# Kernel optimization log

Hardware: AMD Instinct MI355X
Metric: run time of the kernel (lower is better)

Reference implementation:

```python
import jax, jax.numpy as jnp
import numpy as np

B, D, H, W, K = 2, 128, 256, 256, 4
OFFSET_SCALE = 1.0
BN_EPS = 1e-5


def conv2d(x, w, b=None, pad='SAME'):
    y = jax.lax.conv_general_dilated(x, w, (1, 1), pad,
                                     dimension_numbers=('NCHW', 'OIHW', 'NCHW'))
    if b is not None:
        y = y + b[None, :, None, None]
    return y


def grid_sample_border(img, gx, gy):
    # img: (b,d,H,W); gx,gy: (b,K,H,W) normalized coords in [-1,1]
    # bilinear, padding_mode='border', align_corners=True
    b, d, h, w = img.shape
    x = jnp.clip((gx + 1.0) * 0.5 * (w - 1), 0.0, w - 1)
    y = jnp.clip((gy + 1.0) * 0.5 * (h - 1), 0.0, h - 1)
    x0f = jnp.floor(x); y0f = jnp.floor(y)
    wx = x - x0f; wy = y - y0f
    x0 = x0f.astype(jnp.int32); y0 = y0f.astype(jnp.int32)
    x1 = jnp.minimum(x0 + 1, w - 1); y1 = jnp.minimum(y0 + 1, h - 1)
    imgT = jnp.transpose(img, (0, 2, 3, 1))  # (b,H,W,d)
    bidx = jnp.arange(b)[:, None, None, None]  # broadcasts over (b,K,H,W)
    def gather(yi, xi):
        return imgT[bidx, yi, xi]  # (b,K,H,W,d)
    out = (gather(y0, x0) * ((1 - wx) * (1 - wy))[..., None]
           + gather(y0, x1) * (wx * (1 - wy))[..., None]
           + gather(y1, x0) * ((1 - wx) * wy)[..., None]
           + gather(y1, x1) * (wx * wy)[..., None])
    return out  # (b,K,H,W,d)


def setup_inputs() -> dict:
    key = jax.random.key(0)
    ks = jax.random.split(key, 6)
    return {
        'bev': jax.random.normal(ks[0], (B, D, H, W), jnp.float32),
        'offset_w': jax.random.normal(ks[1], (2 * K, D, 3, 3), jnp.float32) * 0.02,
        'offset_b': jax.random.normal(ks[2], (2 * K,), jnp.float32) * 0.02,
        'weight_w': jax.random.normal(ks[3], (K, D, 3, 3), jnp.float32) * 0.05,
        'weight_b': jnp.zeros((K,), jnp.float32),
        'proj_w': jax.random.normal(ks[4], (D, D, 1, 1), jnp.float32) * (1.0 / np.sqrt(D)),
        'bn_gamma': jnp.ones((D,), jnp.float32),
        'bn_beta': jnp.zeros((D,), jnp.float32),
    }


def reference(bev, offset_w, offset_b, weight_w, weight_b, proj_w, bn_gamma, bn_beta):
    b, d, h, w = bev.shape
    # per-pixel K offsets (pixels) and K attention weights
    offsets = conv2d(bev, offset_w, offset_b) * OFFSET_SCALE  # (b,2K,H,W)
    w_logits = conv2d(bev, weight_w, weight_b)                # (b,K,H,W)
    attn = jax.nn.softmax(w_logits, axis=1)                   # softmax over K
    # base grid: replicates torch meshgrid(xy) + transpose (requires H==W)
    xs = jnp.linspace(-1.0, 1.0, w)
    ys = jnp.linspace(-1.0, 1.0, h)
    base_x = xs[:, None] * jnp.ones((1, h), jnp.float32)  # base_x[i,j] = xs[i]
    base_y = jnp.ones((w, 1), jnp.float32) * ys[None, :]  # base_y[i,j] = ys[j]
    off = offsets.reshape(b, K, 2, h, w)
    dx = off[:, :, 0]  # (b,K,H,W)
    dy = off[:, :, 1]
    dx_n = dx * (2.0 / (w - 1)) if w > 1 else dx * 0.0
    dy_n = dy * (2.0 / (h - 1)) if h > 1 else dy * 0.0
    gx = base_x[None, None] + dx_n  # (b,K,H,W)
    gy = base_y[None, None] + dy_n
    sampled = grid_sample_border(bev, gx, gy)  # (b,K,H,W,d)
    aggregated = jnp.einsum('bkhwd,bkhw->bdhw', sampled, attn)
    # proj: 1x1 conv (no bias) + BatchNorm2d (training mode: batch stats) + GELU(exact)
    y = conv2d(aggregated, proj_w)
    mean = jnp.mean(y, axis=(0, 2, 3), keepdims=True)
    var = jnp.mean((y - mean) ** 2, axis=(0, 2, 3), keepdims=True)
    y = (y - mean) * jax.lax.rsqrt(var + BN_EPS)
    y = y * bn_gamma[None, :, None, None] + bn_beta[None, :, None, None]
    return jax.nn.gelu(y, approximate=False)
```

## Files before the change

### kernel.cpp

```cpp
#include <hip/hip_runtime.h>
#include <math.h>

#define BB 2
#define DD 128
#define HH 256
#define WW 256
#define KK 4
#define HWC (HH*WW)
#define SROW2 320

typedef unsigned int u32;
typedef unsigned short ushort;
typedef __attribute__((ext_vector_type(8))) short bf16x8;
typedef __attribute__((ext_vector_type(4))) float f32x4;

#define OA_OFF    0
#define WTT_OFF   1572864
#define WP_OFF    1589248
#define STATS_OFF 1603072
#define PART_OFF  1603392
#define BEVT_OFF  1605440
#define PACC_OFF  18382656
#define PART2_OFF PACC_OFF
#define WBF_OFF   26771264
#define WCB_OFF   26779456
#define WS_NEED_BEVT  ((size_t)PACC_OFF * 4)
#define WS_NEED_FULL3 ((size_t)(WCB_OFF + 9216) * 4)

__device__ __forceinline__ u32 f2bf(float x) {
    u32 u = __builtin_bit_cast(u32, x);
    return (u + 0x7fffu + ((u >> 16) & 1u)) >> 16;
}
__device__ __forceinline__ u32 pkbf(float a, float b) {
    return f2bf(a) | (f2bf(b) << 16);
}
__device__ __forceinline__ float bflo(u32 d) { return __builtin_bit_cast(float, d << 16); }
__device__ __forceinline__ float bfhi(u32 d) { return __builtin_bit_cast(float, d & 0xffff0000u); }

__global__ __launch_bounds__(256) void k0_prep(
    const float* __restrict__ projw, const float* __restrict__ offw,
    const float* __restrict__ wtw, float* __restrict__ wtT, float* __restrict__ wp)
{
    int idx = blockIdx.x * 256 + threadIdx.x;
    if (idx < 16384) {
        int d = idx >> 7, o = idx & 127;
        wtT[d * 128 + o] = projw[o * 128 + d];
    }
    if (idx < 13824) {
        int c = idx / 108; int r = idx % 108; int o = r / 9; int t = r % 9;
        wp[idx] = (o < 8) ? offw[(o*128 + c)*9 + t] : wtw[((o-8)*128 + c)*9 + t];
    }
}

__global__ __launch_bounds__(256) void k0bc(
    const float* __restrict__ projw, const float* __restrict__ offw,
    const float* __restrict__ wtw, ushort* __restrict__ wbf,
    ushort* __restrict__ wcb)
{
    int idx = blockIdx.x * 256 + threadIdx.x;
    if (idx < 16384) wbf[idx] = (ushort)f2bf(projw[idx]);
    if (idx < 18432) {
        int tap = idx >> 11;
        int rem = idx & 2047;
        int oo = rem >> 7, c = rem & 127;
        float v = 0.f;
        if (oo < 8)       v = offw[(oo*128 + c)*9 + tap];
        else if (oo < 12) v = wtw[((oo-8)*128 + c)*9 + tap];
        wcb[idx] = (ushort)f2bf(v);
    }
}

__global__ __launch_bounds__(256) void k2t_bf(
    const float* __restrict__ bev, ushort* __restrict__ bevtb)
{
    __shared__ float T[64 * 128];
    int tid = threadIdx.x;
    int bidx = blockIdx.x;
    int b = bidx >> 10;
    int rem = bidx & 1023;
    int yrow = rem >> 2;
    int x0 = (rem & 3) << 6;

    const float* src = bev + ((size_t)b * DD) * HWC + (size_t)yrow * WW + x0;
    #pragma unroll 4
    for (int k = 0; k < 32; k++) {
        int flat = k * 256 + tid;
        int d = flat >> 6, xl = flat & 63;
        float v = src[(size_t)d * HWC + xl];
        T[xl * 128 + (((d >> 2) ^ (xl & 31)) << 2) + (d & 3)] = v;
    }
    __syncthreads();
    ushort* dst = bevtb + (((size_t)b * HH + yrow) * WW + x0) * 128;
    #pragma unroll 4
    for (int k = 0; k < 8; k++) {
        int flat = k * 256 + tid;
        int d4 = flat & 31, xl = (flat >> 5) & 63;
        float4 v = *(const float4*)&T[xl * 128 + ((d4 ^ (xl & 31)) << 2)];
        uint2 pk;
        pk.x = pkbf(v.x, v.y);
        pk.y = pkbf(v.z, v.w);
        *(uint2*)(dst + (size_t)xl * 128 + (d4 << 2)) = pk;
    }
}

__global__ __launch_bounds__(256) void k1m_conv_mfma(
    const ushort* __restrict__ bevtb, const ushort* __restrict__ wcb,
    const float* __restrict__ offb, const float* __restrict__ wtb,
    float* __restrict__ oa)
{
    __shared__ uint4 lds4[3168];

    int tid = threadIdx.x;
    int wv = tid >> 6;
    int l = tid & 63;
    int lm = l & 15, lk = l >> 4;
    int wgid = blockIdx.x;
    int lin = (wgid & 7) * 256 + (wgid >> 3);
    int b = lin >> 10;
    int i = (lin >> 2) & 255;
    int jt = lin & 3;
    int x0 = jt * 64;

    const ushort* bb = bevtb + (size_t)b * HWC * 128;
    for (int z = tid; z < 3168; z += 256) {
        int row = z / 1056;
        int rem = z - row * 1056;
        int pl = rem >> 4;
        int q  = rem & 15;
        int yy = i - 1 + row;
        int x  = x0 - 1 + pl;
        bool ok = ((unsigned)yy < HH) && ((unsigned)x < WW);
        uint4 v = make_uint4(0u, 0u, 0u, 0u);
        if (ok) v = *(const uint4*)(bb + ((size_t)(yy * WW + x) << 7) + q * 8);
        lds4[row * 1056 + pl * 16 + (q ^ (pl & 15))] = v;
    }
    __syncthreads();

    f32x4 acc = (f32x4)(0.f);
    #pragma unroll
    for (int dy = 0; dy < 3; dy++) {
        #pragma unroll
        for (int dx = 0; dx < 3; dx++) {
            int pl = wv * 16 + lm + dx;
            const uint4* bp = &lds4[dy * 1056 + pl * 16];
            int sx = pl & 15;
            const ushort* ap = wcb + (size_t)((dy*3 + dx) * 16 + lm) * 128 + lk * 8;
            #pragma unroll
            for (int kk = 0; kk < 4; kk++) {
                bf16x8 bfr = *(const bf16x8*)&bp[(kk*4 + lk) ^ sx];
                bf16x8 afr = *(const bf16x8*)(ap + kk * 32);
                acc = __builtin_amdgcn_mfma_f32_16x16x32_bf16(afr, bfr, acc, 0, 0, 0);
            }
        }
    }

    float v[4];
    #pragma unroll
    for (int r = 0; r < 4; r++) v[r] = acc[r];

    int j = x0 + wv * 16 + lm;
    if (lk < 2) {
        #pragma unroll
        for (int r = 0; r < 4; r++) v[r] += offb[lk*4 + r];
    } else if (lk == 2) {
        float l4[4];
        #pragma unroll
        for (int r = 0; r < 4; r++) l4[r] = v[r] + wtb[r];
        float m = fmaxf(fmaxf(l4[0], l4[1]), fmaxf(l4[2], l4[3]));
        float e[4]; float se = 0.f;
        #pragma unroll
        for (int r = 0; r < 4; r++) { e[r] = expf(l4[r] - m); se += e[r]; }
        float inv = 1.f / se;
        #pragma unroll
        for (int r = 0; r < 4; r++) v[r] = e[r] * inv;
    }
    if (lk < 3) {
        size_t basep = (size_t)b * 12 * HWC + (size_t)i * WW + j;
        #pragma unroll
        for (int r = 0; r < 4; r++)
            oa[basep + (size_t)(lk*4 + r) * HWC] = v[r];
    }
}

__global__ __launch_bounds__(256) void k2f_sample_proj(
    const ushort* __restrict__ bevtb, const float* __restrict__ oa,
    const ushort* __restrict__ wbf, float* __restrict__ y,
    float* __restrict__ part2)
{
    __shared__ uint4 P[32 * 16];

    int tid = threadIdx.x;
    int wgid = blockIdx.x;
    int lin = (wgid & 7) * 512 + (wgid >> 3);
    int b = lin >> 11;
    int pix0 = (lin & 2047) << 5;

    int q8 = tid & 7;
    int pixl = tid >> 3;
    int pix = pix0 + pixl;
    int p = pix >> 8;
    int q = pix & 255;

    const float* ob = oa + (size_t)b * 12 * HWC + (size_t)p * WW + q;
    unsigned pa[8]; float cw[16];
    #pragma unroll
    for (int k = 0; k < 4; k++) {
        float dx = ob[(size_t)(2*k)   * HWC];
        float dy = ob[(size_t)(2*k+1) * HWC];
        float a  = ob[(size_t)(8+k)   * HWC];
        float x  = fminf(fmaxf((float)p + dx, 0.f), (float)(WW-1));
        float yv = fminf(fmaxf((float)q + dy, 0.f), (float)(HH-1));
        float x0f = floorf(x); float y0f = floorf(yv);
        int x0 = (int)x0f; int y0 = (int)y0f;
        int x1 = min(x0 + 1, WW - 1); int y1 = min(y0 + 1, HH - 1);
        float wx = x - x0f; float wy = yv - y0f;
        pa[k*2+0] = (unsigned)(y0*WW + x0) | ((unsigned)(y0*WW + x1) << 16);
        pa[k*2+1] = (unsigned)(y1*WW + x0) | ((unsigned)(y1*WW + x1) << 16);
        cw[k*4+0] = a * (1.f - wx) * (1.f - wy);
        cw[k*4+1] = a * wx * (1.f - wy);
        cw[k*4+2] = a * (1.f - wx) * wy;
        cw[k*4+3] = a * wx * wy;
    }

    const ushort* bt = bevtb + (size_t)b * HWC * 128 + q8 * 8;

    float s[2][8];
    #pragma unroll
    for (int c = 0; c < 2; c++)
        #pragma unroll
        for (int e = 0; e < 8; e++) s[c][e] = 0.f;

    #pragma unroll
    for (int t = 0; t < 16; t++) {
        unsigned a01 = pa[t >> 1];
        unsigned gp = (t & 1) ? (a01 >> 16) : (a01 & 0xffffu);
        const ushort* tp = bt + ((size_t)gp << 7);
        float w = cw[t];
        #pragma unroll
        for (int c = 0; c < 2; c++) {
            uint4 v = *(const uint4*)(tp + c * 64);
            s[c][0] = fmaf(w, bflo(v.x), s[c][0]);
            s[c][1] = fmaf(w, bfhi(v.x), s[c][1]);
            s[c][2] = fmaf(w, bflo(v.y), s[c][2]);
            s[c][3] = fmaf(w, bfhi(v.y), s[c][3]);
            s[c][4] = fmaf(w, bflo(v.z), s[c][4]);
            s[c][5] = fmaf(w, bfhi(v.z), s[c][5]);
            s[c][6] = fmaf(w, bflo(v.w), s[c][6]);
            s[c][7] = fmaf(w, bfhi(v.w), s[c][7]);
        }
    }

    int sxr = pixl & 15;
    #pragma unroll
    for (int c = 0; c < 2; c++) {
        uint4 pk;
        pk.x = pkbf(s[c][0], s[c][1]);
        pk.y = pkbf(s[c][2], s[c][3]);
        pk.z = pkbf(s[c][4], s[c][5]);
        pk.w = pkbf(s[c][6], s[c][7]);
        P[pixl * 16 + ((c * 8 + q8) ^ sxr)] = pk;
    }
    __syncthreads();

    int wv = tid >> 6;
    int l = tid & 63;
    int lm = l & 15, lk = l >> 4;
    int o0 = wv << 5;

    f32x4 acc[2][2];
    #pragma unroll
    for (int ot = 0; ot < 2; ot++)
        #pragma unroll
        for (int nt = 0; nt < 2; nt++)
            acc[ot][nt] = (f32x4)(0.f);

    #pragma unroll
    for (int ot = 0; ot < 2; ot++) {
        const ushort* ap = wbf + (size_t)(o0 + ot * 16 + lm) * 128 + lk * 8;
        bf16x8 a4[4];
        #pragma unroll
        for (int kk = 0; kk < 4; kk++)
            a4[kk] = *(const bf16x8*)(ap + kk * 32);
        #pragma unroll
        for (int nt = 0; nt < 2; nt++) {
            int row = nt * 16 + lm;
            #pragma unroll
            for (int kk = 0; kk < 4; kk++) {
                bf16x8 bfr = *(const bf16x8*)&P[row * 16 + ((kk * 4 + lk) ^ lm)];
                acc[ot][nt] = __builtin_amdgcn_mfma_f32_16x16x32_bf16(
                    a4[kk], bfr, acc[ot][nt], 0, 0, 0);
            }
        }
    }

    #pragma unroll
    for (int ot = 0; ot < 2; ot++)
        #pragma unroll
        for (int nt = 0; nt < 2; nt++)
            #pragma unroll
            for (int r = 0; r < 4; r++)
                y[((size_t)b * DD + o0 + ot * 16 + lk * 4 + r) * HWC + pix0 + nt * 16 + lm]
                    = acc[ot][nt][r];

    float sm[2][4], sq[2][4];
    #pragma unroll
    for (int ot = 0; ot < 2; ot++)
        #pragma unroll
        for (int r = 0; r < 4; r++) { sm[ot][r] = 0.f; sq[ot][r] = 0.f; }
    #pragma unroll
    for (int ot = 0; ot < 2; ot++)
        #pragma unroll
        for (int nt = 0; nt < 2; nt++)
            #pragma unroll
            for (int r = 0; r < 4; r++) {
                float v = acc[ot][nt][r];
                sm[ot][r] += v;
                sq[ot][r] = fmaf(v, v, sq[ot][r]);
            }
    #pragma unroll
    for (int m = 1; m < 16; m <<= 1) {
        #pragma unroll
        for (int ot = 0; ot < 2; ot++)
            #pragma unroll
            for (int r = 0; r < 4; r++) {
                sm[ot][r] += __shfl_xor(sm[ot][r], m);
                sq[ot][r] += __shfl_xor(sq[ot][r], m);
            }
    }
    if (lm == 0) {
        #pragma unroll
        for (int ot = 0; ot < 2; ot++)
            #pragma unroll
            for (int r = 0; r < 4; r++) {
                int o = o0 + ot * 16 + lk * 4 + r;
                part2[(size_t)o * 4096 + wgid] = sm[ot][r];
                part2[(size_t)128 * 4096 + (size_t)o * 4096 + wgid] = sq[ot][r];
            }
    }
}

__global__ __launch_bounds__(256) void k3b_finalize2(
    const float* __restrict__ part2, const float* __restrict__ gamma,
    const float* __restrict__ beta, float* __restrict__ stats)
{
    int o = blockIdx.x; int tid = threadIdx.x;
    const float* ps = part2 + (size_t)o * 4096;
    const float* pq = part2 + (size_t)128 * 4096 + (size_t)o * 4096;
    double s = 0.0, s2 = 0.0;
    for (int i = tid; i < 4096; i += 256) { s += (double)ps[i]; s2 += (double)pq[i]; }
    __shared__ double ls[256], ls2[256];
    ls[tid] = s; ls2[tid] = s2;
    __syncthreads();
    for (int off = 128; off > 0; off >>= 1) {
        if (tid < off) { ls[tid] += ls[tid+off]; ls2[tid] += ls2[tid+off]; }
        __syncthreads();
    }
    if (tid == 0) {
        double N = (double)(BB * HWC);
        double mean = ls[0] / N;
        double var = ls2[0] / N - mean * mean;
        double invs = 1.0 / sqrt(var + 1e-5);
        double g = (double)gamma[o];
        stats[o*2]   = (float)(g * invs);
        stats[o*2+1] = (float)((double)beta[o] - mean * g * invs);
    }
}

__global__ __launch_bounds__(256) void k1_convs(
    const float* __restrict__ bev, const float* __restrict__ wp,
    const float* __restrict__ offb, const float* __restrict__ wtb,
    float* __restrict__ oa)
{
    __shared__ float rows[2][3][260];
    int tid = threadIdx.x;
    int p = blockIdx.x;
    int b = p / HH; int i = p % HH; int j = tid;
    const float* bb = bev + (size_t)b * DD * HWC;

    if (tid < 12) { int bf = tid / 6, r = tid % 6; rows[bf][r >> 1][(r & 1) ? 257 : 0] = 0.f; }
    #pragma unroll
    for (int l = 0; l < 3; l++) {
        int yy = i + l - 1;
        rows[0][l][1 + tid] = ((unsigned)yy < HH) ? bb[yy * WW + tid] : 0.f;
    }
    __syncthreads();

    float acc[12];
    #pragma unroll
    for (int o = 0; o < 12; o++) acc[o] = 0.f;

    for (int c = 0; c < 128; c++) {
        int cb = c & 1, nb = cb ^ 1;
        float rv[3];
        if (c < 127) {
            const float* pln = bb + (size_t)(c + 1) * HWC;
            #pragma unroll
            for (int l = 0; l < 3; l++) {
                int yy = i + l - 1;
                rv[l] = ((unsigned)yy < HH) ? pln[yy * WW + tid] : 0.f;
            }
        }
        float v[9];
        #pragma unroll
        for (int dy = 0; dy < 3; dy++)
            #pragma unroll
            for (int dx = 0; dx < 3; dx++)
                v[dy*3 + dx] = rows[cb][dy][tid + dx];
        const float* wc = wp + c * 108;
        #pragma unroll
        for (int o = 0; o < 12; o++) {
            float s = acc[o];
            #pragma unroll
            for (int t = 0; t < 9; t++) s = fmaf(wc[o*9 + t], v[t], s);
            acc[o] = s;
        }
        if (c < 127) {
            #pragma unroll
            for (int l = 0; l < 3; l++) rows[nb][l][1 + tid] = rv[l];
        }
        __syncthreads();
    }

    float outv[12];
    #pragma unroll
    for (int o = 0; o < 8; o++) outv[o] = acc[o] + offb[o];
    float l4[4];
    #pragma unroll
    for (int k = 0; k < 4; k++) l4[k] = acc[8+k] + wtb[k];
    float m = fmaxf(fmaxf(l4[0], l4[1]), fmaxf(l4[2], l4[3]));
    float e[4]; float se = 0.f;
    #pragma unroll
    for (int k = 0; k < 4; k++) { e[k] = expf(l4[k] - m); se += e[k]; }
    float inv = 1.f / se;
    #pragma unroll
    for (int k = 0; k < 4; k++) outv[8+k] = e[k] * inv;

    size_t basep = (size_t)b * 12 * HWC + (size_t)i * WW + j;
    #pragma unroll
    for (int o = 0; o < 12; o++) oa[basep + (size_t)o * HWC] = outv[o];
}

__global__ __launch_bounds__(256) void k2t_transpose(
    const float* __restrict__ bev, float* __restrict__ bevt)
{
    __shared__ float T[64 * 128];
    int tid = threadIdx.x;
    int bidx = blockIdx.x;
    int b = bidx >> 10;
    int rem = bidx & 1023;
    int yrow = rem >> 2;
    int x0 = (rem & 3) << 6;

    const float* src = bev + ((size_t)b * DD) * HWC + (size_t)yrow * WW + x0;
    #pragma unroll 4
    for (int k = 0; k < 32; k++) {
        int flat = k * 256 + tid;
        int d = flat >> 6, xl = flat & 63;
        float v = src[(size_t)d * HWC + xl];
        T[xl * 128 + (((d >> 2) ^ (xl & 31)) << 2) + (d & 3)] = v;
    }
    __syncthreads();
    float* dst = bevt + (((size_t)b * HH + yrow) * WW + x0) * 128;
    #pragma unroll 4
    for (int k = 0; k < 8; k++) {
        int flat = k * 256 + tid;
        int d4 = flat & 31, xl = (flat >> 5) & 63;
        float4 v = *(const float4*)&T[xl * 128 + ((d4 ^ (xl & 31)) << 2)];
        *(float4*)(dst + (size_t)xl * 128 + (d4 << 2)) = v;
    }
}

__global__ __launch_bounds__(512, 2) void k2_sample_proj_t(
    const float* __restrict__ bevt, const float* __restrict__ oa,
    const float* __restrict__ wt, float* __restrict__ y)
{
    __shared__ float S[2][16 * SROW2];

    int tid = threadIdx.x;
    int bidx = blockIdx.x;
    int b  = bidx >> 8;
    int p0 = ((bidx >> 4) & 15) * 16;
    int q0 = (bidx & 15) * 16;

    int gpix = tid >> 1;
    int gp = gpix & 15;
    int gq = gpix >> 4;
    int dgrp = tid & 1;
    int swr = gp * 20 + gq;

    int wv = tid >> 6;
    int wvu = __builtin_amdgcn_readfirstlane(wv);
    int lane = tid & 63;
    int lp = lane >> 2;
    int q4 = (lane & 3) << 2;
    int soff = lp * 20 + q4;

    const float* ob = oa + (size_t)b * 12 * HWC + (size_t)(p0 + gp) * WW + (q0 + gq);
    unsigned pa[8]; float cw[16];
    #pragma unroll
    for (int k = 0; k < 4; k++) {
        float dx = ob[(size_t)(2*k)   * HWC];
        float dy = ob[(size_t)(2*k+1) * HWC];
        float a  = ob[(size_t)(8+k)   * HWC];
        float x  = fminf(fmaxf((float)(p0 + gp) + dx, 0.f), (float)(WW-1));
        float yv = fminf(fmaxf((float)(q0 + gq) + dy, 0.f), (float)(HH-1));
        float x0f = floorf(x); float y0f = floorf(yv);
        int x0 = (int)x0f; int y0 = (int)y0f;
        int x1 = min(x0 + 1, WW - 1); int y1 = min(y0 + 1, HH - 1);
        float wx = x - x0f; float wy = yv - y0f;
        pa[k*2+0] = (unsigned)(y0*WW + x0) | ((unsigned)(y0*WW + x1) << 16);
        pa[k*2+1] = (unsigned)(y1*WW + x0) | ((unsigned)(y1*WW + x1) << 16);
        cw[k*4+0] = a * (1.f - wx) * (1.f - wy);
        cw[k*4+1] = a * wx * (1.f - wy);
        cw[k*4+2] = a * (1.f - wx) * wy;
        cw[k*4+3] = a * wx * wy;
    }

    const float* bt = bevt + (size_t)b * HWC * 128 + dgrp * 8;

    float acc[64];
    #pragma unroll
    for (int t = 0; t < 64; t++) acc[t] = 0.f;

    {
        float4 s0 = make_float4(0,0,0,0), s1 = make_float4(0,0,0,0);
        #pragma unroll
        for (int t = 0; t < 16; t++) {
            unsigned pix = (t & 1) ? (pa[t >> 1] >> 16) : (pa[t >> 1] & 0xffffu);
            const float4* tp = (const float4*)(bt + ((size_t)pix << 7));
            float4 va = tp[0], vb = tp[1];
            float c = cw[t];
            s0.x = fmaf(c, va.x, s0.x); s0.y = fmaf(c, va.y, s0.y);
            s0.z = fmaf(c, va.z, s0.z); s0.w = fmaf(c, va.w, s0.w);
            s1.x = fmaf(c, vb.x, s1.x); s1.y = fmaf(c, vb.y, s1.y);
            s1.z = fmaf(c, vb.z, s1.z); s1.w = fmaf(c, vb.w, s1.w);
        }
        int r = dgrp * 8;
        S[0][(r+0)*SROW2 + swr] = s0.x; S[0][(r+1)*SROW2 + swr] = s0.y;
        S[0][(r+2)*SROW2 + swr] = s0.z; S[0][(r+3)*SROW2 + swr] = s0.w;
        S[0][(r+4)*SROW2 + swr] = s1.x; S[0][(r+5)*SROW2 + swr] = s1.y;
        S[0][(r+6)*SROW2 + swr] = s1.z; S[0][(r+7)*SROW2 + swr] = s1.w;
    }
    __syncthreads();

    for (int c = 0; c < 8; c++) {
        int cur = c & 1;
        const float* Sc = &S[cur][0];
        float* Sn = &S[cur ^ 1][0];
        int d0 = c * 16;
        int dn = d0 + 16;
        bool more = (c < 7);

        float4 g0 = make_float4(0,0,0,0), g1 = make_float4(0,0,0,0);
        float4 pf0, pf1;
        if (more) {
            unsigned pix = pa[0] & 0xffffu;
            const float4* tp = (const float4*)(bt + ((size_t)pix << 7) + dn);
            pf0 = tp[0]; pf1 = tp[1];
        }

        #pragma unroll
        for (int dl = 0; dl < 16; dl++) {
            float4 cur0 = pf0, cur1 = pf1;
            if (more && dl < 15) {
                int t = dl + 1;
                unsigned pix = (t & 1) ? (pa[t >> 1] >> 16) : (pa[t >> 1] & 0xffffu);
                const float4* tp = (const float4*)(bt + ((size_t)pix << 7) + dn);
                pf0 = tp[0]; pf1 = tp[1];
            }

            float4 sv = *(const float4*)(Sc + dl * SROW2 + soff);
            const float4* wq = (const float4*)(wt + (size_t)(d0 + dl) * 128 + wvu * 16);
            #pragma unroll
            for (int oi4 = 0; oi4 < 4; oi4++) {
                float4 w4 = wq[oi4];
                int ob4 = oi4 * 16;
                acc[ob4+ 0] = fmaf(w4.x, sv.x, acc[ob4+ 0]);
                acc[ob4+ 1] = fmaf(w4.x, sv.y, acc[ob4+ 1]);
                acc[ob4+ 2] = fmaf(w4.x, sv.z, acc[ob4+ 2]);
                acc[ob4+ 3] = fmaf(w4.x, sv.w, acc[ob4+ 3]);
                acc[ob4+ 4] = fmaf(w4.y, sv.x, acc[ob4+ 4]);
                acc[ob4+ 5] = fmaf(w4.y, sv.y, acc[ob4+ 5]);
                acc[ob4+ 6] = fmaf(w4.y, sv.z, acc[ob4+ 6]);
                acc[ob4+ 7] = fmaf(w4.y, sv.w, acc[ob4+ 7]);
                acc[ob4+ 8] = fmaf(w4.z, sv.x, acc[ob4+ 8]);
                acc[ob4+ 9] = fmaf(w4.z, sv.y, acc[ob4+ 9]);
                acc[ob4+10] = fmaf(w4.z, sv.z, acc[ob4+10]);
                acc[ob4+11] = fmaf(w4.z, sv.w, acc[ob4+11]);
                acc[ob4+12] = fmaf(w4.w, sv.x, acc[ob4+12]);
                acc[ob4+13] = fmaf(w4.w, sv.y, acc[ob4+13]);
                acc[ob4+14] = fmaf(w4.w, sv.z, acc[ob4+14]);
                acc[ob4+15] = fmaf(w4.w, sv.w, acc[ob4+15]);
            }

            if (more) {
                float cwt = cw[dl];
                g0.x = fmaf(cwt, cur0.x, g0.x); g0.y = fmaf(cwt, cur0.y, g0.y);
                g0.z = fmaf(cwt, cur0.z, g0.z); g0.w = fmaf(cwt, cur0.w, g0.w);
                g1.x = fmaf(cwt, cur1.x, g1.x); g1.y = fmaf(cwt, cur1.y, g1.y);
                g1.z = fmaf(cwt, cur1.z, g1.z); g1.w = fmaf(cwt, cur1.w, g1.w);
            }
        }

        if (more) {
            int r = dgrp * 8;
            Sn[(r+0)*SROW2 + swr] = g0.x; Sn[(r+1)*SROW2 + swr] = g0.y;
            Sn[(r+2)*SROW2 + swr] = g0.z; Sn[(r+3)*SROW2 + swr] = g0.w;
            Sn[(r+4)*SROW2 + swr] = g1.x; Sn[(r+5)*SROW2 + swr] = g1.y;
            Sn[(r+6)*SROW2 + swr] = g1.z; Sn[(r+7)*SROW2 + swr] = g1.w;
        }
        __syncthreads();
    }

    size_t base = (size_t)b * DD * HWC + (size_t)(p0 + lp) * WW + (q0 + q4);
    #pragma unroll
    for (int oi = 0; oi < 16; oi++) {
        int o = wv * 16 + oi;
        float4 v = make_float4(acc[oi*4+0], acc[oi*4+1], acc[oi*4+2], acc[oi*4+3]);
        *(float4*)(y + base + (size_t)o * HWC) = v;
    }
}

__global__ __launch_bounds__(512, 2) void k2_sample_proj(
    const float* __restrict__ bev, const float* __restrict__ oa,
    const float* __restrict__ wt, float* __restrict__ y)
{
    __shared__ float S[2][16 * SROW2];
    int tid = threadIdx.x;
    int bidx = blockIdx.x;
    int b  = bidx >> 8;
    int p0 = ((bidx >> 4) & 15) * 16;
    int q0 = (bidx & 15) * 16;
    int pix = tid & 255;
    int gq = pix >> 4;
    int gp = pix & 15;
    int dgrp = tid >> 8;
    int swr = gp * 20 + gq;
    int wv = tid >> 6;
    int wvu = __builtin_amdgcn_readfirstlane(wv);
    int lane = tid & 63;
    int lp = lane >> 2;
    int q4 = (lane & 3) << 2;
    int soff = lp * 20 + q4;

    const float* ob = oa + (size_t)b * 12 * HWC + (size_t)(p0 + gp) * WW + (q0 + gq);
    unsigned pa[8]; float cw[16];
    #pragma unroll
    for (int k = 0; k < 4; k++) {
        float dx = ob[(size_t)(2*k)   * HWC];
        float dy = ob[(size_t)(2*k+1) * HWC];
        float a  = ob[(size_t)(8+k)   * HWC];
        float x  = fminf(fmaxf((float)(p0 + gp) + dx, 0.f), (float)(WW-1));
        float yv = fminf(fmaxf((float)(q0 + gq) + dy, 0.f), (float)(HH-1));
        float x0f = floorf(x); float y0f = floorf(yv);
        int x0 = (int)x0f; int y0 = (int)y0f;
        int x1 = min(x0 + 1, WW - 1); int y1 = min(y0 + 1, HH - 1);
        float wx = x - x0f; float wy = yv - y0f;
        pa[k*2+0] = (unsigned)(y0*WW + x0) | ((unsigned)(y0*WW + x1) << 16);
        pa[k*2+1] = (unsigned)(y1*WW + x0) | ((unsigned)(y1*WW + x1) << 16);
        cw[k*4+0] = a * (1.f - wx) * (1.f - wy);
        cw[k*4+1] = a * wx * (1.f - wy);
        cw[k*4+2] = a * (1.f - wx) * wy;
        cw[k*4+3] = a * wx * wy;
    }
    const float* bb = bev + (size_t)b * DD * HWC;
    float acc[64];
    #pragma unroll
    for (int t = 0; t < 64; t++) acc[t] = 0.f;
    #pragma unroll
    for (int dd = 0; dd < 8; dd++) {
        const float* pl = bb + (size_t)(dgrp*8 + dd) * HWC;
        float s = 0.f;
        #pragma unroll
        for (int t = 0; t < 8; t++) {
            unsigned a01 = pa[t];
            s = fmaf(cw[2*t],   pl[a01 & 0xffffu], s);
            s = fmaf(cw[2*t+1], pl[a01 >> 16], s);
        }
        S[0][(dgrp*8 + dd) * SROW2 + swr] = s;
    }
    __syncthreads();
    for (int c = 0; c < 8; c++) {
        int cur = c & 1;
        const float* Sc = &S[cur][0];
        float* Sn = &S[cur ^ 1][0];
        int d0 = c * 16;
        int d0n = d0 + 16;
        bool more = (c < 7);
        #pragma unroll
        for (int dl = 0; dl < 16; dl++) {
            if (dl < 8) {
                if (more) {
                    const float* pl = bb + (size_t)(d0n + dgrp*8 + dl) * HWC;
                    float s = 0.f;
                    #pragma unroll
                    for (int t = 0; t < 8; t++) {
                        unsigned a01 = pa[t];
                        s = fmaf(cw[2*t],   pl[a01 & 0xffffu], s);
                        s = fmaf(cw[2*t+1], pl[a01 >> 16], s);
                    }
                    Sn[(dgrp*8 + dl) * SROW2 + swr] = s;
                }
            }
            float4 sv = *(const float4*)(Sc + dl * SROW2 + soff);
            const float4* wq = (const float4*)(wt + (size_t)(d0 + dl) * 128 + wvu * 16);
            #pragma unroll
            for (int oi4 = 0; oi4 < 4; oi4++) {
                float4 w4 = wq[oi4];
                int ob4 = oi4 * 16;
                acc[ob4+ 0] = fmaf(w4.x, sv.x, acc[ob4+ 0]);
                acc[ob4+ 1] = fmaf(w4.x, sv.y, acc[ob4+ 1]);
                acc[ob4+ 2] = fmaf(w4.x, sv.z, acc[ob4+ 2]);
                acc[ob4+ 3] = fmaf(w4.x, sv.w, acc[ob4+ 3]);
                acc[ob4+ 4] = fmaf(w4.y, sv.x, acc[ob4+ 4]);
                acc[ob4+ 5] = fmaf(w4.y, sv.y, acc[ob4+ 5]);
                acc[ob4+ 6] = fmaf(w4.y, sv.z, acc[ob4+ 6]);
                acc[ob4+ 7] = fmaf(w4.y, sv.w, acc[ob4+ 7]);
                acc[ob4+ 8] = fmaf(w4.z, sv.x, acc[ob4+ 8]);
                acc[ob4+ 9] = fmaf(w4.z, sv.y, acc[ob4+ 9]);
                acc[ob4+10] = fmaf(w4.z, sv.z, acc[ob4+10]);
                acc[ob4+11] = fmaf(w4.z, sv.w, acc[ob4+11]);
                acc[ob4+12] = fmaf(w4.w, sv.x, acc[ob4+12]);
                acc[ob4+13] = fmaf(w4.w, sv.y, acc[ob4+13]);
                acc[ob4+14] = fmaf(w4.w, sv.z, acc[ob4+14]);
                acc[ob4+15] = fmaf(w4.w, sv.w, acc[ob4+15]);
            }
        }
        __syncthreads();
    }
    size_t base = (size_t)b * DD * HWC + (size_t)(p0 + lp) * WW + (q0 + q4);
    #pragma unroll
    for (int oi = 0; oi < 16; oi++) {
        int o = wv * 16 + oi;
        float4 v = make_float4(acc[oi*4+0], acc[oi*4+1], acc[oi*4+2], acc[oi*4+3]);
        *(float4*)(y + base + (size_t)o * HWC) = v;
    }
}

__global__ __launch_bounds__(256) void k3_partial(
    const float* __restrict__ y, double* __restrict__ part)
{
    int blk = blockIdx.x;
    int o = blk >> 2; int sub = blk & 3; int b = sub >> 1; int half = sub & 1;
    const float4* pl = (const float4*)(y + ((size_t)b * DD + o) * HWC + half * (HWC/2));
    int tid = threadIdx.x;
    double s = 0.0, s2 = 0.0;
    for (int idx = tid; idx < HWC/8; idx += 256) {
        float4 v = pl[idx];
        s  += (double)v.x + (double)v.y + (double)v.z + (double)v.w;
        s2 += (double)v.x*v.x + (double)v.y*v.y + (double)v.z*v.z + (double)v.w*v.w;
    }
    __shared__ double ls[256], ls2[256];
    ls[tid] = s; ls2[tid] = s2;
    __syncthreads();
    for (int off = 128; off > 0; off >>= 1) {
        if (tid < off) { ls[tid] += ls[tid+off]; ls2[tid] += ls2[tid+off]; }
        __syncthreads();
    }
    if (tid == 0) { part[blk*2] = ls[0]; part[blk*2+1] = ls2[0]; }
}

__global__ __launch_bounds__(128) void k3_finalize(
    const double* __restrict__ part, const float* __restrict__ gamma,
    const float* __restrict__ beta, float* __restrict__ stats)
{
    int o = threadIdx.x;
    double s = 0.0, s2 = 0.0;
    #pragma unroll
    for (int j = 0; j < 4; j++) { s += part[(o*4+j)*2]; s2 += part[(o*4+j)*2+1]; }
    double N = (double)(BB * HWC);
    double mean = s / N;
    double var = s2 / N - mean * mean;
    double invs = 1.0 / sqrt(var + 1e-5);
    double g = (double)gamma[o];
    stats[o*2]   = (float)(g * invs);
    stats[o*2+1] = (float)((double)beta[o] - mean * g * invs);
}

__global__ __launch_bounds__(256) void k4_bn_gelu(
    float* __restrict__ y, const float* __restrict__ stats)
{
    size_t idx4 = (size_t)blockIdx.x * 256 + threadIdx.x;
    float4* p = (float4*)y;
    float4 v = p[idx4];
    int o = (int)((idx4 * 4) / HWC) % DD;
    float sc = stats[o*2], sh = stats[o*2+1];
    const float inv_sqrt2 = 0.70710678118654752f;
    float g0 = fmaf(v.x, sc, sh);
    float g1 = fmaf(v.y, sc, sh);
    float g2 = fmaf(v.z, sc, sh);
    float g3 = fmaf(v.w, sc, sh);
    v.x = 0.5f * g0 * (1.f + erff(g0 * inv_sqrt2));
    v.y = 0.5f * g1 * (1.f + erff(g1 * inv_sqrt2));
    v.z = 0.5f * g2 * (1.f + erff(g2 * inv_sqrt2));
    v.w = 0.5f * g3 * (1.f + erff(g3 * inv_sqrt2));
    p[idx4] = v;
}

extern "C" void kernel_launch(void* const* d_in, const int* in_sizes, int n_in,
                              void* d_out, int out_size, void* d_ws, size_t ws_size,
                              hipStream_t stream) {
    const float* bev   = (const float*)d_in[0];
    const float* offw  = (const float*)d_in[1];
    const float* offb  = (const float*)d_in[2];
    const float* wtw   = (const float*)d_in[3];
    const float* wtb   = (const float*)d_in[4];
    const float* projw = (const float*)d_in[5];
    const float* gamma = (const float*)d_in[6];
    const float* beta  = (const float*)d_in[7];
    float* out = (float*)d_out;
    float* wsf = (float*)d_ws;

    float* oa    = wsf + OA_OFF;
    float* wtT   = wsf + WTT_OFF;
    float* wp    = wsf + WP_OFF;
    float* stats = wsf + STATS_OFF;
    double* part = (double*)(wsf + PART_OFF);
    float* bevt  = wsf + BEVT_OFF;
    ushort* bevtb = (ushort*)(wsf + BEVT_OFF);
    ushort* wbf  = (ushort*)(wsf + WBF_OFF);
    ushort* wcb  = (ushort*)(wsf + WCB_OFF);
    float* part2 = wsf + PART2_OFF;

    bool full3 = ws_size >= WS_NEED_FULL3;
    bool big   = ws_size >= WS_NEED_BEVT;

    if (full3) {
        hipLaunchKernelGGL(k0bc, dim3(72), dim3(256), 0, stream,
                           projw, offw, wtw, wbf, wcb);
        hipLaunchKernelGGL(k2t_bf, dim3(2048), dim3(256), 0, stream, bev, bevtb);
        hipLaunchKernelGGL(k1m_conv_mfma, dim3(2048), dim3(256), 0, stream,
                           bevtb, wcb, offb, wtb, oa);
        hipLaunchKernelGGL(k2f_sample_proj, dim3(4096), dim3(256), 0, stream,
                           bevtb, oa, wbf, out, part2);
        hipLaunchKernelGGL(k3b_finalize2, dim3(128), dim3(256), 0, stream,
                           part2, gamma, beta, stats);
    } else if (big) {
        hipLaunchKernelGGL(k0_prep, dim3(64), dim3(256), 0, stream,
                           projw, offw, wtw, wtT, wp);
        hipLaunchKernelGGL(k2t_transpose, dim3(2048), dim3(256), 0, stream, bev, bevt);
        hipLaunchKernelGGL(k1_convs, dim3(BB*HH), dim3(256), 0, stream,
                           bev, wp, offb, wtb, oa);
        hipLaunchKernelGGL(k2_sample_proj_t, dim3(BB*256), dim3(512), 0, stream,
                           bevt, oa, wtT, out);
        hipLaunchKernelGGL(k3_partial, dim3(512), dim3(256), 0, stream, out, part);
        hipLaunchKernelGGL(k3_finalize, dim3(1), dim3(128), 0, stream,
                           part, gamma, beta, stats);
    } else {
        hipLaunchKernelGGL(k0_prep, dim3(64), dim3(256), 0, stream,
                           projw, offw, wtw, wtT, wp);
        hipLaunchKernelGGL(k1_convs, dim3(BB*HH), dim3(256), 0, stream,
                           bev, wp, offb, wtb, oa);
        hipLaunchKernelGGL(k2_sample_proj, dim3(BB*256), dim3(512), 0, stream,
                           bev, oa, wtT, out);
        hipLaunchKernelGGL(k3_partial, dim3(512), dim3(256), 0, stream, out, part);
        hipLaunchKernelGGL(k3_finalize, dim3(1), dim3(128), 0, stream,
                           part, gamma, beta, stats);
    }
    hipLaunchKernelGGL(k4_bn_gelu, dim3((BB*DD*HWC)/1024), dim3(256), 0, stream,
                       out, stats);
}
```

Baseline: 160.6 us.

## Shrink conv tiles, batch gather loads in sampler, transpose partial-stat layout

The MFMA conv kernel now uses 128-thread blocks covering 32-pixel row segments, which shrinks shared memory and doubles the grid to raise occupancy. The sampling kernel issues all 16 tap loads up front, keeping more memory requests in flight, and requests 4 blocks per CU through launch bounds. Partial BN statistics are now written contiguously per workgroup rather than strided per channel, and the finalize kernel reads them strided instead. More live registers for the batched loads could force spills or limit occupancy, and the halo-load overhead per tile rises with the smaller conv tiles.

```diff
diff --git a/kernel.cpp b/kernel.cpp
--- a/kernel.cpp
+++ b/kernel.cpp
@@ -103,28 +103,28 @@
     }
 }
 
-__global__ __launch_bounds__(256) void k1m_conv_mfma(
+__global__ __launch_bounds__(128) void k1m_conv_mfma(
     const ushort* __restrict__ bevtb, const ushort* __restrict__ wcb,
     const float* __restrict__ offb, const float* __restrict__ wtb,
     float* __restrict__ oa)
 {
-    __shared__ uint4 lds4[3168];
+    __shared__ uint4 lds4[1632];
 
     int tid = threadIdx.x;
     int wv = tid >> 6;
     int l = tid & 63;
     int lm = l & 15, lk = l >> 4;
     int wgid = blockIdx.x;
-    int lin = (wgid & 7) * 256 + (wgid >> 3);
-    int b = lin >> 10;
-    int i = (lin >> 2) & 255;
-    int jt = lin & 3;
-    int x0 = jt * 64;
+    int lin = (wgid & 7) * 512 + (wgid >> 3);
+    int b = lin >> 11;
+    int i = (lin >> 3) & 255;
+    int jt = lin & 7;
+    int x0 = jt * 32;
 
     const ushort* bb = bevtb + (size_t)b * HWC * 128;
-    for (int z = tid; z < 3168; z += 256) {
-        int row = z / 1056;
-        int rem = z - row * 1056;
+    for (int z = tid; z < 1632; z += 128) {
+        int row = z / 544;
+        int rem = z - row * 544;
         int pl = rem >> 4;
         int q  = rem & 15;
         int yy = i - 1 + row;
@@ -132,7 +132,7 @@
         bool ok = ((unsigned)yy < HH) && ((unsigned)x < WW);
         uint4 v = make_uint4(0u, 0u, 0u, 0u);
         if (ok) v = *(const uint4*)(bb + ((size_t)(yy * WW + x) << 7) + q * 8);
-        lds4[row * 1056 + pl * 16 + (q ^ (pl & 15))] = v;
+        lds4[row * 544 + pl * 16 + (q ^ (pl & 15))] = v;
     }
     __syncthreads();
 
@@ -142,7 +142,7 @@
         #pragma unroll
         for (int dx = 0; dx < 3; dx++) {
             int pl = wv * 16 + lm + dx;
-            const uint4* bp = &lds4[dy * 1056 + pl * 16];
+            const uint4* bp = &lds4[dy * 544 + pl * 16];
             int sx = pl & 15;
             const ushort* ap = wcb + (size_t)((dy*3 + dx) * 16 + lm) * 128 + lk * 8;
             #pragma unroll
@@ -182,7 +182,15 @@
     }
 }
 
-__global__ __launch_bounds__(256) void k2f_sample_proj(
+#define TAPPTR(t) (bt + ((size_t)((((t) & 1) ? (pa[(t) >> 1] >> 16) : (pa[(t) >> 1] & 0xffffu))) << 7))
+#define FMA8(S, V, W) do { \
+    S[0] = fmaf(W, bflo((V).x), S[0]); S[1] = fmaf(W, bfhi((V).x), S[1]); \
+    S[2] = fmaf(W, bflo((V).y), S[2]); S[3] = fmaf(W, bfhi((V).y), S[3]); \
+    S[4] = fmaf(W, bflo((V).z), S[4]); S[5] = fmaf(W, bfhi((V).z), S[5]); \
+    S[6] = fmaf(W, bflo((V).w), S[6]); S[7] = fmaf(W, bfhi((V).w), S[7]); \
+} while (0)
+
+__global__ __launch_bounds__(256, 4) void k2f_sample_proj(
     const ushort* __restrict__ bevtb, const float* __restrict__ oa,
     const ushort* __restrict__ wbf, float* __restrict__ y,
     float* __restrict__ part2)
@@ -230,25 +238,27 @@
         #pragma unroll
         for (int e = 0; e < 8; e++) s[c][e] = 0.f;
 
-    #pragma unroll
-    for (int t = 0; t < 16; t++) {
-        unsigned a01 = pa[t >> 1];
-        unsigned gp = (t & 1) ? (a01 >> 16) : (a01 & 0xffffu);
-        const ushort* tp = bt + ((size_t)gp << 7);
-        float w = cw[t];
-        #pragma unroll
-        for (int c = 0; c < 2; c++) {
-            uint4 v = *(const uint4*)(tp + c * 64);
-            s[c][0] = fmaf(w, bflo(v.x), s[c][0]);
-            s[c][1] = fmaf(w, bfhi(v.x), s[c][1]);
-            s[c][2] = fmaf(w, bflo(v.y), s[c][2]);
-            s[c][3] = fmaf(w, bfhi(v.y), s[c][3]);
-            s[c][4] = fmaf(w, bflo(v.z), s[c][4]);
-            s[c][5] = fmaf(w, bfhi(v.z), s[c][5]);
-            s[c][6] = fmaf(w, bflo(v.w), s[c][6]);
-            s[c][7] = fmaf(w, bfhi(v.w), s[c][7]);
-        }
-    }
+    uint4 L0[8], L1[8];
+    #pragma unroll
+    for (int t = 0; t < 8; t++) L0[t] = *(const uint4*)(TAPPTR(t));
+    #pragma unroll
+    for (int t = 0; t < 8; t++) L1[t] = *(const uint4*)(TAPPTR(t + 8));
+    #pragma unroll
+    for (int t = 0; t < 8; t++) {
+        uint4 v = L0[t];
+        L0[t] = *(const uint4*)(TAPPTR(t) + 64);
+        FMA8(s[0], v, cw[t]);
+    }
+    #pragma unroll
+    for (int t = 0; t < 8; t++) {
+        uint4 v = L1[t];
+        L1[t] = *(const uint4*)(TAPPTR(t + 8) + 64);
+        FMA8(s[0], v, cw[t + 8]);
+    }
+    #pragma unroll
+    for (int t = 0; t < 8; t++) FMA8(s[1], L0[t], cw[t]);
+    #pragma unroll
+    for (int t = 0; t < 8; t++) FMA8(s[1], L1[t], cw[t + 8]);
 
     int sxr = pixl & 15;
     #pragma unroll
@@ -328,13 +338,14 @@
             }
     }
     if (lm == 0) {
+        float* pw = part2 + (size_t)wgid * 256;
         #pragma unroll
         for (int ot = 0; ot < 2; ot++)
             #pragma unroll
             for (int r = 0; r < 4; r++) {
                 int o = o0 + ot * 16 + lk * 4 + r;
-                part2[(size_t)o * 4096 + wgid] = sm[ot][r];
-                part2[(size_t)128 * 4096 + (size_t)o * 4096 + wgid] = sq[ot][r];
+                pw[o] = sm[ot][r];
+                pw[128 + o] = sq[ot][r];
             }
     }
 }
@@ -344,10 +355,11 @@
     const float* __restrict__ beta, float* __restrict__ stats)
 {
     int o = blockIdx.x; int tid = threadIdx.x;
-    const float* ps = part2 + (size_t)o * 4096;
-    const float* pq = part2 + (size_t)128 * 4096 + (size_t)o * 4096;
     double s = 0.0, s2 = 0.0;
-    for (int i = tid; i < 4096; i += 256) { s += (double)ps[i]; s2 += (double)pq[i]; }
+    for (int w = tid; w < 4096; w += 256) {
+        s  += (double)part2[(size_t)w * 256 + o];
+        s2 += (double)part2[(size_t)w * 256 + 128 + o];
+    }
     __shared__ double ls[256], ls2[256];
     ls[tid] = s; ls2[tid] = s2;
     __syncthreads();
@@ -829,7 +841,7 @@
         hipLaunchKernelGGL(k0bc, dim3(72), dim3(256), 0, stream,
                            projw, offw, wtw, wbf, wcb);
         hipLaunchKernelGGL(k2t_bf, dim3(2048), dim3(256), 0, stream, bev, bevtb);
-        hipLaunchKernelGGL(k1m_conv_mfma, dim3(2048), dim3(256), 0, stream,
+        hipLaunchKernelGGL(k1m_conv_mfma, dim3(4096), dim3(128), 0, stream,
                            bevtb, wcb, offb, wtb, oa);
         hipLaunchKernelGGL(k2f_sample_proj, dim3(4096), dim3(256), 0, stream,
                            bevtb, oa, wbf, out, part2);
```

New measurement: 156.3 us. -2.7%, faster.
